# Optimization experiments

Hardware: AMD Instinct MI355X
Metric: run time of the kernel (lower is better)

Reference implementation:

```python
import jax, jax.numpy as jnp
from jax import lax
import numpy as np

EPS = 1e-9

def squash(x):
    # squash along last axis: ||x||^2/(1+||x||^2) * x/||x||
    mag_sq = jnp.sum(x * x, axis=-1, keepdims=True)
    mag = jnp.sqrt(mag_sq + EPS)
    return mag_sq / (1.0 + mag_sq) * (x / (mag + EPS))

def setup_inputs() -> dict:
    key = jax.random.key(0)
    ks = jax.random.split(key, 4)
    x = jax.random.normal(ks[0], (64, 1, 64, 64), jnp.float32)
    conv1_w = jax.random.normal(ks[1], (64, 1, 5, 5), jnp.float32) * 0.1
    conv1_b = jnp.zeros((64,), jnp.float32)
    prim_w = jax.random.normal(ks[2], (64, 64, 9, 9), jnp.float32) * 0.05
    prim_b = jnp.zeros((64,), jnp.float32)
    # DigitCaps W: (num_routes=8*28*28, num_caps=10, out_dim=16, in_dim=8); torch uses randn
    W = jax.random.normal(ks[3], (6272, 10, 16, 8), jnp.float32)
    return {"x": x, "conv1_w": conv1_w, "conv1_b": conv1_b,
            "prim_w": prim_w, "prim_b": prim_b, "W": W}

def reference(x, conv1_w, conv1_b, prim_w, prim_b, W):
    dn = ("NCHW", "OIHW", "NCHW")
    # ConvLayer: conv(1->64, k5, pad2) + relu, spatial preserved
    h = lax.conv_general_dilated(x, conv1_w, (1, 1), [(2, 2), (2, 2)], dimension_numbers=dn)
    h = jax.nn.relu(h + conv1_b[None, :, None, None])
    # PrimaryCaps: 8 convs (64->8, k9, s2) fused as one 64-channel conv
    u = lax.conv_general_dilated(h, prim_w, (2, 2), "VALID", dimension_numbers=dn)
    u = u + prim_b[None, :, None, None]  # (B, 64, 28, 28)
    B, _, H, Wd = u.shape
    # (B, caps=8, dim=8, H, W) -> (B, caps, H, W, dim) -> (B, caps*H*W, 8)
    u = u.reshape(B, 8, 8, H, Wd).transpose(0, 1, 3, 4, 2).reshape(B, -1, 8)
    u = squash(u)
    # u_hat[b,n,o,i] = W[n,o,i,j] @ u[b,n,j]   (B, routes, 10, 16)
    u_hat = jnp.einsum("noij,bnj->bnoi", W, u)
    b_ij = jnp.zeros(u_hat.shape[:3], u_hat.dtype)  # (B, routes, 10)
    v = None
    for it in range(3):
        c = jax.nn.softmax(b_ij, axis=2)
        s = jnp.einsum("bno,bnoi->boi", c, u_hat)  # (B, 10, 16)
        v = squash(s)
        if it < 2:
            b_ij = b_ij + jnp.einsum("bnoi,boi->bno", u_hat, v)
    return v.reshape(B, -1)  # (B, 160)
```

## Files before the change

### kernel.cpp

```cpp
#include <hip/hip_runtime.h>
#include <math.h>

typedef unsigned short ushort_t;
typedef __attribute__((ext_vector_type(8))) short bf16x8;
typedef __attribute__((ext_vector_type(4))) float f32x4;
typedef __attribute__((ext_vector_type(8))) unsigned short us8;

typedef __attribute__((address_space(1))) unsigned int gu32;
typedef __attribute__((address_space(3))) unsigned int lu32;

__device__ __forceinline__ void gload16(const void* g, void* l) {
    __builtin_amdgcn_global_load_lds((const gu32*)g, (lu32*)l, 16, 0, 0);
}

__device__ __forceinline__ unsigned short f2bf(float f) {
    unsigned u = __float_as_uint(f);
    unsigned r = ((u >> 16) & 1u) + 0x7fffu;
    return (unsigned short)((u + r) >> 16);
}

#define HB_OFF    0ULL
#define WT2_OFF   8388608ULL
#define UTB_OFF   11765760ULL
#define V0_OFF    13381632ULL
#define V1_OFF    13391872ULL
#define PART_OFF  13402112ULL
#define PART2_OFF 21430272ULL
#define WB2_OFF   21594112ULL

__global__ __launch_bounds__(256) void conv1_nhwc_kernel(const float* __restrict__ x,
                                                         const float* __restrict__ w,
                                                         const float* __restrict__ bias,
                                                         ushort_t* __restrict__ hb) {
    int t = blockIdx.x * 256 + threadIdx.x;
    int xx = t & 63, yy = (t >> 6) & 63, b = t >> 12;
    int cg = blockIdx.y;
    const float* xb = x + (size_t)b * 4096;
    float xv[25];
    #pragma unroll
    for (int ky = 0; ky < 5; ++ky) {
        int iy = yy + ky - 2;
        #pragma unroll
        for (int kx = 0; kx < 5; ++kx) {
            int ix = xx + kx - 2;
            bool ok = (iy >= 0 && iy < 64 && ix >= 0 && ix < 64);
            xv[ky * 5 + kx] = ok ? xb[iy * 64 + ix] : 0.f;
        }
    }
    us8 o;
    #pragma unroll
    for (int cc = 0; cc < 8; ++cc) {
        int c = cg * 8 + cc;
        float acc = bias[c];
        const float* wc = w + c * 25;
        #pragma unroll
        for (int k = 0; k < 25; ++k) acc = fmaf(xv[k], wc[k], acc);
        o[cc] = f2bf(fmaxf(acc, 0.f));
    }
    *(us8*)&hb[(size_t)t * 64 + cg * 8] = o;
}

__global__ __launch_bounds__(256) void prep_weights_kernel(const float* __restrict__ pw,
                                                           const float* __restrict__ W,
                                                           ushort_t* __restrict__ wt2,
                                                           ushort_t* __restrict__ Wb) {
    int bid = blockIdx.x;
    int tid = threadIdx.x;
    if (bid < 1296) {
        int t = bid * 256 + tid;
        int ic = t & 63, c = (t >> 6) & 63, p = t >> 12;
        wt2[t] = f2bf(pw[(size_t)(c * 64 + ic) * 81 + p]);
    } else {
        int t = (bid - 1296) * 256 + tid;
        const float* src = W + (size_t)t * 8;
        us8 o;
        #pragma unroll
        for (int j = 0; j < 8; ++j) o[j] = f2bf(src[j]);
        *(us8*)&Wb[(size_t)t * 8] = o;
    }
}

__global__ __launch_bounds__(256) void conv2_mfma_kernel(const ushort_t* __restrict__ hb,
                                                         const ushort_t* __restrict__ wt2,
                                                         const float* __restrict__ pb,
                                                         ushort_t* __restrict__ utb) {
    __shared__ ushort_t As[2][4096];
    __shared__ ushort_t Bs[2][4096];

    int tid = threadIdx.x;
    int w = tid >> 6, lane = tid & 63;
    int m0 = blockIdx.x * 64;

    int srow = w * 16 + (lane >> 3);
    int srcchunk = (lane & 7) ^ ((lane >> 3) & 7);
    unsigned gbaseA[2];
    #pragma unroll
    for (int k = 0; k < 2; ++k) {
        int r = srow + k * 8;
        int m = m0 + r;
        int b = m / 784, pos = m % 784;
        int oy = pos / 28, ox = pos % 28;
        gbaseA[k] = ((unsigned)((b * 64 + 2 * oy) * 64 + 2 * ox)) * 64 + srcchunk * 8;
    }
    unsigned gbaseB[2] = { (unsigned)srow * 64 + srcchunk * 8,
                           (unsigned)(srow + 8) * 64 + srcchunk * 8 };

    int fr = lane & 15, fq = lane >> 4;
    int rlow = fr & 7;
    int c0 = (fq ^ rlow) * 8;
    int c1 = ((4 + fq) ^ rlow) * 8;
    int rowA = w * 16 + fr;
    int offA0 = rowA * 64 + c0, offA1 = rowA * 64 + c1;
    int offB0[4], offB1[4];
    #pragma unroll
    for (int jf = 0; jf < 4; ++jf) {
        int rowB = jf * 16 + fr;
        offB0[jf] = rowB * 64 + c0;
        offB1[jf] = rowB * 64 + c1;
    }

    f32x4 acc[4] = {};

    auto stage = [&](int p, int buf) {
        int ky = p / 9, kx = p % 9;
        unsigned koff = (unsigned)(ky * 4096 + kx * 64);
        unsigned boff = (unsigned)p * 4096;
        gload16(hb + gbaseA[0] + koff, &As[buf][w * 1024]);
        gload16(hb + gbaseA[1] + koff, &As[buf][w * 1024 + 512]);
        gload16(wt2 + boff + gbaseB[0], &Bs[buf][w * 1024]);
        gload16(wt2 + boff + gbaseB[1], &Bs[buf][w * 1024 + 512]);
    };

    stage(0, 0);
    __syncthreads();

    for (int p = 0; p < 81; ++p) {
        int cur = p & 1;
        if (p < 80) stage(p + 1, cur ^ 1);
        const ushort_t* A = As[cur];
        const ushort_t* B = Bs[cur];
        bf16x8 a0 = *(const bf16x8*)&A[offA0];
        bf16x8 a1 = *(const bf16x8*)&A[offA1];
        bf16x8 b0[4], b1[4];
        #pragma unroll
        for (int jf = 0; jf < 4; ++jf) {
            b0[jf] = *(const bf16x8*)&B[offB0[jf]];
            b1[jf] = *(const bf16x8*)&B[offB1[jf]];
        }
        #pragma unroll
        for (int jf = 0; jf < 4; ++jf)
            acc[jf] = __builtin_amdgcn_mfma_f32_16x16x32_bf16(a0, b0[jf], acc[jf], 0, 0, 0);
        #pragma unroll
        for (int jf = 0; jf < 4; ++jf)
            acc[jf] = __builtin_amdgcn_mfma_f32_16x16x32_bf16(a1, b1[jf], acc[jf], 0, 0, 0);
        __syncthreads();
    }

    float bv[4];
    #pragma unroll
    for (int jf = 0; jf < 4; ++jf) bv[jf] = pb[jf * 16 + fr];

    #pragma unroll
    for (int reg = 0; reg < 4; ++reg) {
        int m = m0 + w * 16 + fq * 4 + reg;
        int bb = m / 784, pos = m % 784;
        #pragma unroll
        for (int jf = 0; jf < 4; ++jf) {
            float val = acc[jf][reg] + bv[jf];
            float v2 = val * val;
            v2 += __shfl_xor(v2, 1);
            v2 += __shfl_xor(v2, 2);
            v2 += __shfl_xor(v2, 4);
            float mag = sqrtf(v2 + 1e-9f);
            float sc = v2 / (1.f + v2) / (mag + 1e-9f);
            int g = jf * 2 + (fr >> 3);
            int j = fr & 7;
            utb[(size_t)((g * 784 + pos) * 64 + bb) * 8 + j] = f2bf(val * sc);
        }
    }
}

#define RPB 8
__global__ __launch_bounds__(256) void routing_iter0_kernel(const ushort_t* __restrict__ Wb,
                                                            const ushort_t* __restrict__ utb,
                                                            float* __restrict__ part) {
    __shared__ ushort_t Wl[RPB * 1280];
    __shared__ ushort_t Ul[RPB * 512];
    int tid = threadIdx.x;
    int lane = tid & 63;
    int wid = tid >> 6;
    int fr = lane & 15, fq = lane >> 4;
    int n0 = blockIdx.x * RPB;

    {
        int w64 = wid * 64;
        const ushort_t* wsrc = Wb + (size_t)n0 * 1280;
        #pragma unroll
        for (int k = 0; k < 5; ++k)
            gload16(wsrc + (size_t)(k * 256 + tid) * 8, &Wl[(k * 256 + w64) * 8]);
        const ushort_t* usrc = utb + (size_t)n0 * 512;
        #pragma unroll
        for (int k = 0; k < 2; ++k)
            gload16(usrc + (size_t)(k * 256 + tid) * 8, &Ul[(k * 256 + w64) * 8]);
    }
    __syncthreads();

    f32x4 s4[10] = {};
    #pragma unroll
    for (int g = 0; g < 2; ++g) {
        int t = g * 4 + fq;
        bf16x8 bfrag = *(const bf16x8*)&Ul[(t * 64 + wid * 16 + fr) * 8];
        #pragma unroll
        for (int o = 0; o < 10; ++o) {
            bf16x8 afrag = *(const bf16x8*)&Wl[(t * 160 + o * 16 + fr) * 8];
            s4[o] = __builtin_amdgcn_mfma_f32_16x16x32_bf16(afrag, bfrag, s4[o], 0, 0, 0);
        }
    }

    float* pp = part + (size_t)blockIdx.x * 10240;
    int b = wid * 16 + fr;
    #pragma unroll
    for (int o = 0; o < 10; ++o)
        #pragma unroll
        for (int r = 0; r < 4; ++r)
            pp[(o * 16 + fq * 4 + r) * 64 + b] = s4[o][r];
}

template<int ITER>
__global__ __launch_bounds__(256) void routing5_kernel(const ushort_t* __restrict__ Wb,
                                                       const ushort_t* __restrict__ utb,
                                                       const float* __restrict__ v0,
                                                       const float* __restrict__ v1,
                                                       float* __restrict__ part) {
    __shared__ ushort_t Wl[RPB * 1280];
    __shared__ ushort_t Ul[RPB * 512];
    int tid = threadIdx.x;
    int lane = tid & 63;
    int wid = tid >> 6;
    int fr = lane & 15, fq = lane >> 4;
    int n0 = blockIdx.x * RPB;
    int b = wid * 16 + fr;

    {
        int w64 = wid * 64;
        const ushort_t* wsrc = Wb + (size_t)n0 * 1280;
        #pragma unroll
        for (int k = 0; k < 5; ++k)
            gload16(wsrc + (size_t)(k * 256 + tid) * 8, &Wl[(k * 256 + w64) * 8]);
        const ushort_t* usrc = utb + (size_t)n0 * 512;
        #pragma unroll
        for (int k = 0; k < 2; ++k)
            gload16(usrc + (size_t)(k * 256 + tid) * 8, &Ul[(k * 256 + w64) * 8]);
    }

    float vsum[40];
    #pragma unroll
    for (int o = 0; o < 10; ++o) {
        f32x4 a = *(const f32x4*)&v0[b * 160 + o * 16 + fq * 4];
        if (ITER == 2) {
            f32x4 cc = *(const f32x4*)&v1[b * 160 + o * 16 + fq * 4];
            a = a + cc;
        }
        *(f32x4*)&vsum[o * 4] = a;
    }

    __syncthreads();

    float sacc[40];
    #pragma unroll
    for (int q = 0; q < 40; ++q) sacc[q] = 0.f;

    const bf16x8 zf = {};
    const f32x4 zc = {};

    #pragma unroll 1
    for (int t = 0; t < RPB; ++t) {
        bf16x8 bfrag = zf;
        if (fq == 0) bfrag = *(const bf16x8*)&Ul[(t * 64 + b) * 8];

        f32x4 uh[10];
        #pragma unroll
        for (int o = 0; o < 10; ++o) {
            bf16x8 afrag = zf;
            if (fq == 0) afrag = *(const bf16x8*)&Wl[(t * 160 + o * 16 + fr) * 8];
            uh[o] = __builtin_amdgcn_mfma_f32_16x16x32_bf16(afrag, bfrag, zc, 0, 0, 0);
        }

        float c10[10];
        {
            float l[10];
            #pragma unroll
            for (int o = 0; o < 10; ++o) {
                float lo = uh[o][0] * vsum[o * 4] + uh[o][1] * vsum[o * 4 + 1] +
                           uh[o][2] * vsum[o * 4 + 2] + uh[o][3] * vsum[o * 4 + 3];
                lo += __shfl_xor(lo, 16);
                lo += __shfl_xor(lo, 32);
                l[o] = lo;
            }
            float m = l[0];
            #pragma unroll
            for (int o = 1; o < 10; ++o) m = fmaxf(m, l[o]);
            float sum = 0.f;
            #pragma unroll
            for (int o = 0; o < 10; ++o) { c10[o] = __expf(l[o] - m); sum += c10[o]; }
            float inv = 1.f / sum;
            #pragma unroll
            for (int o = 0; o < 10; ++o) c10[o] *= inv;
        }

        #pragma unroll
        for (int o = 0; o < 10; ++o) {
            float co = c10[o];
            sacc[o * 4 + 0] = fmaf(co, uh[o][0], sacc[o * 4 + 0]);
            sacc[o * 4 + 1] = fmaf(co, uh[o][1], sacc[o * 4 + 1]);
            sacc[o * 4 + 2] = fmaf(co, uh[o][2], sacc[o * 4 + 2]);
            sacc[o * 4 + 3] = fmaf(co, uh[o][3], sacc[o * 4 + 3]);
        }
    }

    float* pp = part + (size_t)blockIdx.x * 10240;
    #pragma unroll
    for (int o = 0; o < 10; ++o)
        #pragma unroll
        for (int r = 0; r < 4; ++r)
            pp[(o * 16 + fq * 4 + r) * 64 + b] = sacc[o * 4 + r];
}

__global__ __launch_bounds__(256) void reduce_part1_kernel(const float* __restrict__ part,
                                                           float* __restrict__ part2) {
    int idx = blockIdx.x * 256 + threadIdx.x;
    int kc = blockIdx.y;
    const float* p = part + (size_t)kc * 49 * 10240 + idx;
    float a0 = 0.f, a1 = 0.f, a2 = 0.f, a3 = 0.f;
    #pragma unroll
    for (int k = 0; k < 48; k += 4) {
        a0 += p[(size_t)(k + 0) * 10240];
        a1 += p[(size_t)(k + 1) * 10240];
        a2 += p[(size_t)(k + 2) * 10240];
        a3 += p[(size_t)(k + 3) * 10240];
    }
    part2[kc * 10240 + idx] = ((a0 + a1) + (a2 + a3)) + p[48ULL * 10240];
}

__global__ __launch_bounds__(256) void reduce_squash_kernel(const float* __restrict__ part2,
                                                            float scale,
                                                            float* __restrict__ v) {
    __shared__ float sv[16][17];
    int tid = threadIdx.x;
    int o = blockIdx.x;
    int i = tid >> 4, bl = tid & 15;
    int b = blockIdx.y * 16 + bl;
    int idx = (o * 16 + i) * 64 + b;
    float a0 = 0.f, a1 = 0.f, a2 = 0.f, a3 = 0.f;
    #pragma unroll
    for (int k = 0; k < 16; k += 4) {
        a0 += part2[(k + 0) * 10240 + idx];
        a1 += part2[(k + 1) * 10240 + idx];
        a2 += part2[(k + 2) * 10240 + idx];
        a3 += part2[(k + 3) * 10240 + idx];
    }
    float s = ((a0 + a1) + (a2 + a3)) * scale;
    sv[i][bl] = s * s;
    __syncthreads();
    float msq = 0.f;
    #pragma unroll
    for (int ii = 0; ii < 16; ++ii) msq += sv[ii][bl];
    float mag = sqrtf(msq + 1e-9f);
    float sc = msq / (1.f + msq) / (mag + 1e-9f);
    v[b * 160 + o * 16 + i] = s * sc;
}

extern "C" void kernel_launch(void* const* d_in, const int* in_sizes, int n_in,
                              void* d_out, int out_size, void* d_ws, size_t ws_size,
                              hipStream_t stream) {
    const float* x  = (const float*)d_in[0];
    const float* w1 = (const float*)d_in[1];
    const float* b1 = (const float*)d_in[2];
    const float* pw = (const float*)d_in[3];
    const float* pb = (const float*)d_in[4];
    const float* W  = (const float*)d_in[5];
    float* out = (float*)d_out;
    float* ws  = (float*)d_ws;

    ushort_t* hb    = (ushort_t*)(ws + HB_OFF);
    ushort_t* wt2   = (ushort_t*)(ws + WT2_OFF);
    ushort_t* utb   = (ushort_t*)(ws + UTB_OFF);
    float*    v0    = ws + V0_OFF;
    float*    v1    = ws + V1_OFF;
    float*    part  = ws + PART_OFF;
    float*    part2 = ws + PART2_OFF;
    ushort_t* Wb    = (ushort_t*)(ws + WB2_OFF);

    prep_weights_kernel<<<5216, 256, 0, stream>>>(pw, W, wt2, Wb);
    conv1_nhwc_kernel<<<dim3(1024, 8), 256, 0, stream>>>(x, w1, b1, hb);
    conv2_mfma_kernel<<<784, 256, 0, stream>>>(hb, wt2, pb, utb);

    routing_iter0_kernel<<<784, 256, 0, stream>>>(Wb, utb, part);
    reduce_part1_kernel<<<dim3(40, 16), 256, 0, stream>>>(part, part2);
    reduce_squash_kernel<<<dim3(10, 4), 256, 0, stream>>>(part2, 0.1f, v0);

    routing5_kernel<1><<<784, 256, 0, stream>>>(Wb, utb, v0, nullptr, part);
    reduce_part1_kernel<<<dim3(40, 16), 256, 0, stream>>>(part, part2);
    reduce_squash_kernel<<<dim3(10, 4), 256, 0, stream>>>(part2, 1.f, v1);

    routing5_kernel<2><<<784, 256, 0, stream>>>(Wb, utb, v0, v1, part);
    reduce_part1_kernel<<<dim3(40, 16), 256, 0, stream>>>(part, part2);
    reduce_squash_kernel<<<dim3(10, 4), 256, 0, stream>>>(part2, 1.f, out);
}
```

Measured before the change: 290.1 us.

## Merge conv1 and weight prep launches; triple-buffer conv2 with one barrier per tap

Combines the conv1 and weight-conversion kernels into one launch, which saves a launch and lets the two independent jobs overlap. Changes the conv2 MFMA loop from double to triple LDS buffering. It waits on the vector-memory counter so the next tap's loads stay in flight, and uses one raw s_barrier per tap instead of the trailing __syncthreads. This raises LDS use per block and depends on the hand-written waitcnt matching the four async loads per stage.

```diff
diff --git a/kernel.cpp b/kernel.cpp
--- a/kernel.cpp
+++ b/kernel.cpp
@@ -28,50 +28,49 @@
 #define PART2_OFF 21430272ULL
 #define WB2_OFF   21594112ULL
 
-__global__ __launch_bounds__(256) void conv1_nhwc_kernel(const float* __restrict__ x,
-                                                         const float* __restrict__ w,
-                                                         const float* __restrict__ bias,
-                                                         ushort_t* __restrict__ hb) {
-    int t = blockIdx.x * 256 + threadIdx.x;
-    int xx = t & 63, yy = (t >> 6) & 63, b = t >> 12;
-    int cg = blockIdx.y;
-    const float* xb = x + (size_t)b * 4096;
-    float xv[25];
-    #pragma unroll
-    for (int ky = 0; ky < 5; ++ky) {
-        int iy = yy + ky - 2;
-        #pragma unroll
-        for (int kx = 0; kx < 5; ++kx) {
-            int ix = xx + kx - 2;
-            bool ok = (iy >= 0 && iy < 64 && ix >= 0 && ix < 64);
-            xv[ky * 5 + kx] = ok ? xb[iy * 64 + ix] : 0.f;
-        }
-    }
-    us8 o;
-    #pragma unroll
-    for (int cc = 0; cc < 8; ++cc) {
-        int c = cg * 8 + cc;
-        float acc = bias[c];
-        const float* wc = w + c * 25;
-        #pragma unroll
-        for (int k = 0; k < 25; ++k) acc = fmaf(xv[k], wc[k], acc);
-        o[cc] = f2bf(fmaxf(acc, 0.f));
-    }
-    *(us8*)&hb[(size_t)t * 64 + cg * 8] = o;
-}
-
-__global__ __launch_bounds__(256) void prep_weights_kernel(const float* __restrict__ pw,
-                                                           const float* __restrict__ W,
-                                                           ushort_t* __restrict__ wt2,
-                                                           ushort_t* __restrict__ Wb) {
+__global__ __launch_bounds__(256) void pre_kernel(const float* __restrict__ x,
+                                                  const float* __restrict__ w,
+                                                  const float* __restrict__ bias,
+                                                  const float* __restrict__ pw,
+                                                  const float* __restrict__ W,
+                                                  ushort_t* __restrict__ hb,
+                                                  ushort_t* __restrict__ wt2,
+                                                  ushort_t* __restrict__ Wb) {
     int bid = blockIdx.x;
     int tid = threadIdx.x;
-    if (bid < 1296) {
-        int t = bid * 256 + tid;
+    if (bid < 8192) {
+        int t = (bid & 1023) * 256 + tid;
+        int cg = bid >> 10;
+        int xx = t & 63, yy = (t >> 6) & 63, b = t >> 12;
+        const float* xb = x + (size_t)b * 4096;
+        float xv[25];
+        #pragma unroll
+        for (int ky = 0; ky < 5; ++ky) {
+            int iy = yy + ky - 2;
+            #pragma unroll
+            for (int kx = 0; kx < 5; ++kx) {
+                int ix = xx + kx - 2;
+                bool ok = (iy >= 0 && iy < 64 && ix >= 0 && ix < 64);
+                xv[ky * 5 + kx] = ok ? xb[iy * 64 + ix] : 0.f;
+            }
+        }
+        us8 o;
+        #pragma unroll
+        for (int cc = 0; cc < 8; ++cc) {
+            int c = cg * 8 + cc;
+            float acc = bias[c];
+            const float* wc = w + c * 25;
+            #pragma unroll
+            for (int k = 0; k < 25; ++k) acc = fmaf(xv[k], wc[k], acc);
+            o[cc] = f2bf(fmaxf(acc, 0.f));
+        }
+        *(us8*)&hb[(size_t)t * 64 + cg * 8] = o;
+    } else if (bid < 8192 + 1296) {
+        int t = (bid - 8192) * 256 + tid;
         int ic = t & 63, c = (t >> 6) & 63, p = t >> 12;
         wt2[t] = f2bf(pw[(size_t)(c * 64 + ic) * 81 + p]);
     } else {
-        int t = (bid - 1296) * 256 + tid;
+        int t = (bid - 8192 - 1296) * 256 + tid;
         const float* src = W + (size_t)t * 8;
         us8 o;
         #pragma unroll
@@ -84,8 +83,8 @@
                                                          const ushort_t* __restrict__ wt2,
                                                          const float* __restrict__ pb,
                                                          ushort_t* __restrict__ utb) {
-    __shared__ ushort_t As[2][4096];
-    __shared__ ushort_t Bs[2][4096];
+    __shared__ ushort_t As[3][4096];
+    __shared__ ushort_t Bs[3][4096];
 
     int tid = threadIdx.x;
     int w = tid >> 6, lane = tid & 63;
@@ -121,24 +120,20 @@
 
     f32x4 acc[4] = {};
 
-    auto stage = [&](int p, int buf) {
+    auto stage = [&](int p) {
+        int slot = p % 3;
         int ky = p / 9, kx = p % 9;
         unsigned koff = (unsigned)(ky * 4096 + kx * 64);
         unsigned boff = (unsigned)p * 4096;
-        gload16(hb + gbaseA[0] + koff, &As[buf][w * 1024]);
-        gload16(hb + gbaseA[1] + koff, &As[buf][w * 1024 + 512]);
-        gload16(wt2 + boff + gbaseB[0], &Bs[buf][w * 1024]);
-        gload16(wt2 + boff + gbaseB[1], &Bs[buf][w * 1024 + 512]);
+        gload16(hb + gbaseA[0] + koff, &As[slot][w * 1024]);
+        gload16(hb + gbaseA[1] + koff, &As[slot][w * 1024 + 512]);
+        gload16(wt2 + boff + gbaseB[0], &Bs[slot][w * 1024]);
+        gload16(wt2 + boff + gbaseB[1], &Bs[slot][w * 1024 + 512]);
     };
 
-    stage(0, 0);
-    __syncthreads();
-
-    for (int p = 0; p < 81; ++p) {
-        int cur = p & 1;
-        if (p < 80) stage(p + 1, cur ^ 1);
-        const ushort_t* A = As[cur];
-        const ushort_t* B = Bs[cur];
+    auto tap = [&](int p) {
+        const ushort_t* A = As[p % 3];
+        const ushort_t* B = Bs[p % 3];
         bf16x8 a0 = *(const bf16x8*)&A[offA0];
         bf16x8 a1 = *(const bf16x8*)&A[offA1];
         bf16x8 b0[4], b1[4];
@@ -153,7 +148,20 @@
         #pragma unroll
         for (int jf = 0; jf < 4; ++jf)
             acc[jf] = __builtin_amdgcn_mfma_f32_16x16x32_bf16(a1, b1[jf], acc[jf], 0, 0, 0);
-        __syncthreads();
+    };
+
+    stage(0);
+
+    for (int p = 0; p < 81; ++p) {
+        if (p < 80) {
+            stage(p + 1);
+            asm volatile("s_waitcnt vmcnt(4)" ::: "memory");
+        } else {
+            asm volatile("s_waitcnt vmcnt(0)" ::: "memory");
+        }
+        __builtin_amdgcn_s_barrier();
+        __builtin_amdgcn_sched_barrier(0);
+        tap(p);
     }
 
     float bv[4];
@@ -391,8 +399,7 @@
     float*    part2 = ws + PART2_OFF;
     ushort_t* Wb    = (ushort_t*)(ws + WB2_OFF);
 
-    prep_weights_kernel<<<5216, 256, 0, stream>>>(pw, W, wt2, Wb);
-    conv1_nhwc_kernel<<<dim3(1024, 8), 256, 0, stream>>>(x, w1, b1, hb);
+    pre_kernel<<<13408, 256, 0, stream>>>(x, w1, b1, pw, W, hb, wt2, Wb);
     conv2_mfma_kernel<<<784, 256, 0, stream>>>(hb, wt2, pb, utb);
 
     routing_iter0_kernel<<<784, 256, 0, stream>>>(Wb, utb, part);
```

Result: slower. 305.5 us (+5.3%).
